# Kernel tuning notes

Hardware: AMD Instinct MI355X
Metric: run time of the kernel (lower is better)

The kernel has to match this reference:

```python
import jax, jax.numpy as jnp
import numpy as np

P, B, H, IN, L = 64, 256, 512, 2, 2


def setup_inputs() -> dict:
    key = jax.random.key(0)
    ks = jax.random.split(key, 16)
    s = 1.0 / np.sqrt(H)
    inp = {
        'input_traces': jax.random.normal(ks[0], (B, P, IN), jnp.float32),
        'h0': jax.random.normal(ks[1], (P, L, B, H), jnp.float32) * 0.1,
        'c0': jax.random.normal(ks[2], (P, L, B, H), jnp.float32) * 0.1,
        # layer 0 LSTM params (PyTorch layout: [4H, in] with gate order i,f,g,o)
        'w_ih0': jax.random.uniform(ks[3], (4 * H, IN), jnp.float32, -s, s),
        'w_hh0': jax.random.uniform(ks[4], (4 * H, H), jnp.float32, -s, s),
        'b_ih0': jax.random.uniform(ks[5], (4 * H,), jnp.float32, -s, s),
        'b_hh0': jax.random.uniform(ks[6], (4 * H,), jnp.float32, -s, s),
        # layer 1 LSTM params
        'w_ih1': jax.random.uniform(ks[7], (4 * H, H), jnp.float32, -s, s),
        'w_hh1': jax.random.uniform(ks[8], (4 * H, H), jnp.float32, -s, s),
        'b_ih1': jax.random.uniform(ks[9], (4 * H,), jnp.float32, -s, s),
        'b_hh1': jax.random.uniform(ks[10], (4 * H,), jnp.float32, -s, s),
    }
    return inp


def _lstm_forward(input_traces, h0, c0, params):
    # Fuse pedestrian and batch dims into one big batch PB = P*B; the original
    # loops over pedestrians calling the SAME LSTM weights, so this is exact.
    x = jnp.transpose(input_traces, (1, 0, 2)).reshape(P * B, IN)  # [PB, 2]
    h = jnp.transpose(h0, (1, 0, 2, 3)).reshape(L, P * B, H)       # [L, PB, H]
    c = jnp.transpose(c0, (1, 0, 2, 3)).reshape(L, P * B, H)
    h_next, c_next = [], []
    for l in range(L):
        wi, wh, bi, bh = params[l]
        gates = x @ wi.T + bi + h[l] @ wh.T + bh                   # [PB, 4H]
        ig, fg, gg, og = jnp.split(gates, 4, axis=-1)
        ig, fg, og = jax.nn.sigmoid(ig), jax.nn.sigmoid(fg), jax.nn.sigmoid(og)
        gg = jnp.tanh(gg)
        c_new = fg * c[l] + ig * gg
        h_new = og * jnp.tanh(c_new)
        h_next.append(h_new)
        c_next.append(c_new)
        x = h_new
    out = x.reshape(P, B, H).transpose(1, 0, 2)                    # [B, P, H]
    hn = jnp.stack(h_next).reshape(L, P, B, H).transpose(1, 0, 2, 3)
    cn = jnp.stack(c_next).reshape(L, P, B, H).transpose(1, 0, 2, 3)
    return out, hn, cn


def reference(input_traces, h0, c0, w_ih0, w_hh0, b_ih0, b_hh0,
              w_ih1, w_hh1, b_ih1, b_hh1):
    params = [(w_ih0, w_hh0, b_ih0, b_hh0), (w_ih1, w_hh1, b_ih1, b_hh1)]
    return _lstm_forward(input_traces, h0, c0, params)
```

## Files before the change

kernel.cpp:

```cpp
#include <hip/hip_runtime.h>
#include <hip/hip_bf16.h>

#define PP 64
#define BB 256
#define HH 512
#define MM (PP * BB)

#define HN_BASE (BB * PP * HH)
#define CN_BASE (HN_BASE + PP * 2 * BB * HH)

typedef __attribute__((ext_vector_type(8))) short bf16x8;
typedef __attribute__((ext_vector_type(4))) float floatx4;

__device__ __forceinline__ float sigf(float x) { return 1.0f / (1.0f + __expf(-x)); }
__device__ __forceinline__ float tanh_(float x) { return 2.0f / (1.0f + __expf(-2.0f * x)) - 1.0f; }

__device__ __forceinline__ short f2bf(float f) {
  unsigned u = __float_as_uint(f);
  u = (u + 0x7FFFu + ((u >> 16) & 1u)) >> 16;
  return (short)u;
}

template <typename T>
__device__ __forceinline__ float tofl(T v);
template <> __device__ __forceinline__ float tofl<float>(float v) { return v; }
template <> __device__ __forceinline__ float tofl<__hip_bfloat16>(__hip_bfloat16 v) { return __bfloat162float(v); }

template <typename T>
__device__ __forceinline__ T fromfl(float v);
template <> __device__ __forceinline__ float fromfl<float>(float v) { return v; }
template <> __device__ __forceinline__ __hip_bfloat16 fromfl<__hip_bfloat16>(float v) { return __float2bfloat16(v); }

template <typename T>
__device__ __forceinline__ bf16x8 load8(const T* p);
template <> __device__ __forceinline__ bf16x8 load8<__hip_bfloat16>(const __hip_bfloat16* p) {
  return *(const bf16x8*)p;
}
template <> __device__ __forceinline__ bf16x8 load8<float>(const float* p) {
  float4 f0 = *(const float4*)p;
  float4 f1 = *((const float4*)p + 1);
  bf16x8 v;
  v[0] = f2bf(f0.x); v[1] = f2bf(f0.y); v[2] = f2bf(f0.z); v[3] = f2bf(f0.w);
  v[4] = f2bf(f1.x); v[5] = f2bf(f1.y); v[6] = f2bf(f1.z); v[7] = f2bf(f1.w);
  return v;
}

__device__ __forceinline__ bool detect_f32(const void* w_ih0) {
  const unsigned short* p = (const unsigned short*)w_ih0;
  int l = threadIdx.x & 63;
  unsigned short a = p[2 * l], b = p[2 * l + 1];
  int big = ((a & 0x7F80) >= 0x3F80) || ((b & 0x7F80) >= 0x3F80);
  return __any(big);
}

template <typename T, int LAYER>
__device__ __forceinline__ void lstm_body(
    const T* __restrict__ xin, const T* __restrict__ h0, const T* __restrict__ c0,
    const T* __restrict__ wih, const T* __restrict__ whh,
    const T* __restrict__ bih, const T* __restrict__ bhh,
    T* out, __hip_bfloat16* ldsA, __hip_bfloat16* ldsW)
{
  const int tid  = threadIdx.x;
  const int nb   = blockIdx.x;
  const int hb   = blockIdx.y;
  const int lane = tid & 63;
  const int wid  = tid >> 6;
  const int quad = lane >> 4;
  const int lrow = lane & 15;
  const int p0   = nb >> 1;

  floatx4 acc[4][4];
#pragma unroll
  for (int g = 0; g < 4; ++g)
#pragma unroll
    for (int mi = 0; mi < 4; ++mi)
#pragma unroll
      for (int q = 0; q < 4; ++q) acc[g][mi][q] = 0.0f;

  int arow[4], wrow[4];
#pragma unroll
  for (int mi = 0; mi < 4; ++mi) arow[mi] = (wid >> 1) * 64 + mi * 16 + lrow;
#pragma unroll
  for (int g = 0; g < 4; ++g) wrow[g] = g * 32 + (wid & 1) * 16 + lrow;

  const int sr = tid >> 3;
  const int sc = tid & 7;

  const int KITERS = (LAYER == 0) ? 8 : 16;

  for (int kt = 0; kt < KITERS; ++kt) {
    bf16x8 ra[4], rw[4];
#pragma unroll
    for (int round = 0; round < 4; ++round) {
      int r = sr + round * 32;
      int b = ((nb & 1) << 7) + r;
      const T* srcA;
      if (LAYER == 0) {
        srcA = h0 + ((size_t)((p0 * 2) * 256 + b)) * 512 + kt * 64 + sc * 8;
      } else {
        if (kt < 8)
          srcA = out + HN_BASE + ((size_t)((p0 * 2) * 256 + b)) * 512 + kt * 64 + sc * 8;
        else
          srcA = h0 + ((size_t)((p0 * 2 + 1) * 256 + b)) * 512 + (kt - 8) * 64 + sc * 8;
      }
      ra[round] = load8<T>(srcA);

      int j = (r >> 5) * 512 + hb * 32 + (r & 31);
      const T* srcW;
      if (LAYER == 0) {
        srcW = whh + (size_t)j * 512 + kt * 64 + sc * 8;
      } else {
        if (kt < 8) srcW = wih + (size_t)j * 512 + kt * 64 + sc * 8;
        else        srcW = whh + (size_t)j * 512 + (kt - 8) * 64 + sc * 8;
      }
      rw[round] = load8<T>(srcW);
    }

    __syncthreads();
#pragma unroll
    for (int round = 0; round < 4; ++round) {
      int r = sr + round * 32;
      int p = sc ^ (r & 7);
      *(bf16x8*)((char*)ldsA + r * 128 + p * 16) = ra[round];
      *(bf16x8*)((char*)ldsW + r * 128 + p * 16) = rw[round];
    }
    __syncthreads();

#pragma unroll
    for (int ks = 0; ks < 2; ++ks) {
      bf16x8 aF[4], wF[4];
#pragma unroll
      for (int mi = 0; mi < 4; ++mi) {
        int ch = (ks * 4 + quad) ^ (arow[mi] & 7);
        aF[mi] = *(const bf16x8*)((const char*)ldsA + arow[mi] * 128 + ch * 16);
      }
#pragma unroll
      for (int g = 0; g < 4; ++g) {
        int ch = (ks * 4 + quad) ^ (wrow[g] & 7);
        wF[g] = *(const bf16x8*)((const char*)ldsW + wrow[g] * 128 + ch * 16);
      }
#pragma unroll
      for (int g = 0; g < 4; ++g)
#pragma unroll
        for (int mi = 0; mi < 4; ++mi)
          acc[g][mi] = __builtin_amdgcn_mfma_f32_16x16x32_bf16(
              aF[mi], wF[g], acc[g][mi], 0, 0, 0);
    }
  }

  const int hloc = hb * 32 + (wid & 1) * 16 + lrow;
  float bias[4], wx0[4], wx1[4];
#pragma unroll
  for (int g = 0; g < 4; ++g) {
    int j = g * 512 + hloc;
    bias[g] = tofl<T>(bih[j]) + tofl<T>(bhh[j]);
    if (LAYER == 0) {
      wx0[g] = tofl<T>(wih[j * 2]);
      wx1[g] = tofl<T>(wih[j * 2 + 1]);
    }
  }
  const int crow0 = (p0 * 2 + LAYER) * 256;
#pragma unroll
  for (int mi = 0; mi < 4; ++mi) {
#pragma unroll
    for (int r = 0; r < 4; ++r) {
      int b = ((nb & 1) << 7) + (wid >> 1) * 64 + mi * 16 + quad * 4 + r;
      float gv0 = acc[0][mi][r] + bias[0];
      float gv1 = acc[1][mi][r] + bias[1];
      float gv2 = acc[2][mi][r] + bias[2];
      float gv3 = acc[3][mi][r] + bias[3];
      if (LAYER == 0) {
        float x0 = tofl<T>(xin[(b * 64 + p0) * 2]);
        float x1 = tofl<T>(xin[(b * 64 + p0) * 2 + 1]);
        gv0 += x0 * wx0[0] + x1 * wx1[0];
        gv1 += x0 * wx0[1] + x1 * wx1[1];
        gv2 += x0 * wx0[2] + x1 * wx1[2];
        gv3 += x0 * wx0[3] + x1 * wx1[3];
      }
      float ig = sigf(gv0), fg = sigf(gv1);
      float gg = tanh_(gv2), og = sigf(gv3);
      size_t ro = ((size_t)(crow0 + b)) * 512 + hloc;
      float co   = tofl<T>(c0[ro]);
      float cnew = fg * co + ig * gg;
      float hnew = og * tanh_(cnew);
      out[HN_BASE + ro] = fromfl<T>(hnew);
      out[CN_BASE + ro] = fromfl<T>(cnew);
      if (LAYER == 1)
        out[(size_t)(b * 64 + p0) * 512 + hloc] = fromfl<T>(hnew);
    }
  }
}

template <int LAYER>
__global__ void __launch_bounds__(256)
lstm_layer(const void* xin, const void* h0, const void* c0,
           const void* wih, const void* whh, const void* bih, const void* bhh,
           const void* w_ih0_detect, void* out)
{
  __shared__ __align__(16) __hip_bfloat16 ldsA[128 * 64];
  __shared__ __align__(16) __hip_bfloat16 ldsW[128 * 64];
  if (detect_f32(w_ih0_detect)) {
    lstm_body<float, LAYER>((const float*)xin, (const float*)h0, (const float*)c0,
                            (const float*)wih, (const float*)whh,
                            (const float*)bih, (const float*)bhh,
                            (float*)out, ldsA, ldsW);
  } else {
    lstm_body<__hip_bfloat16, LAYER>((const __hip_bfloat16*)xin, (const __hip_bfloat16*)h0,
                                     (const __hip_bfloat16*)c0, (const __hip_bfloat16*)wih,
                                     (const __hip_bfloat16*)whh, (const __hip_bfloat16*)bih,
                                     (const __hip_bfloat16*)bhh, (__hip_bfloat16*)out,
                                     ldsA, ldsW);
  }
}

extern "C" void kernel_launch(void* const* d_in, const int* in_sizes, int n_in,
                              void* d_out, int out_size, void* d_ws, size_t ws_size,
                              hipStream_t stream) {
  dim3 grid(MM / 128, HH / 32);
  dim3 block(256);
  lstm_layer<0><<<grid, block, 0, stream>>>(d_in[0], d_in[1], d_in[2],
                                            d_in[3], d_in[4], d_in[5], d_in[6],
                                            d_in[3], d_out);
  lstm_layer<1><<<grid, block, 0, stream>>>(d_in[0], d_in[1], d_in[2],
                                            d_in[7], d_in[8], d_in[9], d_in[10],
                                            d_in[3], d_out);
}
```

Baseline: 523.4 us.

## Pre-pack h0 and weights into bf16 swizzled tiles in workspace

Adds prep kernels that convert h0 and the recurrent/input weights to bf16 and lay them out as contiguous pre-swizzled 16KB tiles in the workspace. The GEMM kernels then read those tiles directly, coalesced and without per-iteration fp32-to-bf16 conversion, and prefetch the next k-tile into registers while the current one is computed. Layer 0 also writes its h output as bf16 straight into the tile layout layer 1 consumes. This removes repeated fp32 loads and conversions across the 16 h-blocks, at the cost of two extra launches and workspace traffic; the new path only runs if the workspace is large enough.

```diff
diff --git a/kernel.cpp b/kernel.cpp
--- a/kernel.cpp
+++ b/kernel.cpp
@@ -8,6 +8,15 @@
 
 #define HN_BASE (BB * PP * HH)
 #define CN_BASE (HN_BASE + PP * 2 * BB * HH)
+
+#define TILE_BYTES 16384
+#define WS_A0   0ull
+#define WS_A1A  16777216ull
+#define WS_A1B  33554432ull
+#define WS_W0   50331648ull
+#define WS_W1A  52428800ull
+#define WS_W1B  54525952ull
+#define WS_NEED 56623104ull
 
 typedef __attribute__((ext_vector_type(8))) short bf16x8;
 typedef __attribute__((ext_vector_type(4))) float floatx4;
@@ -51,6 +60,229 @@
   unsigned short a = p[2 * l], b = p[2 * l + 1];
   int big = ((a & 0x7F80) >= 0x3F80) || ((b & 0x7F80) >= 0x3F80);
   return __any(big);
+}
+
+
+template <typename T>
+__device__ __forceinline__ void prep_A_body(const T* __restrict__ h0, char* __restrict__ ws) {
+  const int pb = blockIdx.x, kt = blockIdx.y, l = blockIdx.z;
+  char* dst = ws + (l ? WS_A1B : WS_A0) + ((size_t)(pb * 8 + kt)) * TILE_BYTES;
+  const int ped = pb >> 1, bh = pb & 1;
+  const T* src = h0 + ((size_t)(ped * 2 + l) * 256) * 512;
+  const int tid = threadIdx.x;
+#pragma unroll
+  for (int i = 0; i < 4; ++i) {
+    int idx = i * 256 + tid;
+    int r = idx >> 3;
+    int p = idx & 7;
+    int c = p ^ (r & 7);
+    *(bf16x8*)(dst + (size_t)idx * 16) =
+        load8<T>(src + (size_t)(bh * 128 + r) * 512 + kt * 64 + c * 8);
+  }
+}
+
+__global__ void __launch_bounds__(256) prep_A_k(const void* h0, const void* det, void* ws) {
+  if (detect_f32(det)) prep_A_body<float>((const float*)h0, (char*)ws);
+  else prep_A_body<__hip_bfloat16>((const __hip_bfloat16*)h0, (char*)ws);
+}
+
+template <typename T>
+__device__ __forceinline__ void prep_W_body(const T* __restrict__ w0, const T* __restrict__ w1a,
+                                            const T* __restrict__ w1b, char* __restrict__ ws) {
+  const int m = blockIdx.x >> 4, hb = blockIdx.x & 15, kt = blockIdx.y;
+  const T* src = (m == 0) ? w0 : (m == 1 ? w1a : w1b);
+  const size_t base = (m == 0) ? WS_W0 : (m == 1 ? WS_W1A : WS_W1B);
+  char* dst = ws + base + ((size_t)(hb * 8 + kt)) * TILE_BYTES;
+  const int tid = threadIdx.x;
+#pragma unroll
+  for (int i = 0; i < 4; ++i) {
+    int idx = i * 256 + tid;
+    int r = idx >> 3;
+    int p = idx & 7;
+    int c = p ^ (r & 7);
+    int j = (r >> 5) * 512 + hb * 32 + (r & 31);
+    *(bf16x8*)(dst + (size_t)idx * 16) =
+        load8<T>(src + (size_t)j * 512 + kt * 64 + c * 8);
+  }
+}
+
+__global__ void __launch_bounds__(256) prep_W_k(const void* w0, const void* w1a, const void* w1b,
+                                                const void* det, void* ws) {
+  if (detect_f32(det)) prep_W_body<float>((const float*)w0, (const float*)w1a, (const float*)w1b, (char*)ws);
+  else prep_W_body<__hip_bfloat16>((const __hip_bfloat16*)w0, (const __hip_bfloat16*)w1a,
+                                   (const __hip_bfloat16*)w1b, (char*)ws);
+}
+
+template <typename T, int LAYER>
+__device__ __forceinline__ void lstm_ws_body(
+    const T* __restrict__ xin, const T* __restrict__ c0,
+    const T* __restrict__ wih, const T* __restrict__ bih, const T* __restrict__ bhh,
+    T* __restrict__ out, char* __restrict__ ws,
+    char* __restrict__ ldsA, char* __restrict__ ldsW)
+{
+  const int tid  = threadIdx.x;
+  const int nb   = blockIdx.x;
+  const int hb   = blockIdx.y;
+  const int lane = tid & 63;
+  const int wid  = tid >> 6;
+  const int quad = lane >> 4;
+  const int lrow = lane & 15;
+  const int p0   = nb >> 1;
+
+  floatx4 acc[4][4];
+#pragma unroll
+  for (int g = 0; g < 4; ++g)
+#pragma unroll
+    for (int mi = 0; mi < 4; ++mi)
+#pragma unroll
+      for (int q = 0; q < 4; ++q) acc[g][mi][q] = 0.0f;
+
+  int arow[4], wrow[4];
+#pragma unroll
+  for (int mi = 0; mi < 4; ++mi) arow[mi] = (wid >> 1) * 64 + mi * 16 + lrow;
+#pragma unroll
+  for (int g = 0; g < 4; ++g) wrow[g] = g * 32 + (wid & 1) * 16 + lrow;
+
+  constexpr int KITERS = (LAYER == 0) ? 8 : 16;
+
+  auto tileptr = [&](int kt, const char*& at, const char*& wt) {
+    if (LAYER == 0) {
+      at = ws + WS_A0  + ((size_t)(nb * 8 + kt)) * TILE_BYTES;
+      wt = ws + WS_W0  + ((size_t)(hb * 8 + kt)) * TILE_BYTES;
+    } else if (kt < 8) {
+      at = ws + WS_A1A + ((size_t)(nb * 8 + kt)) * TILE_BYTES;
+      wt = ws + WS_W1A + ((size_t)(hb * 8 + kt)) * TILE_BYTES;
+    } else {
+      at = ws + WS_A1B + ((size_t)(nb * 8 + kt - 8)) * TILE_BYTES;
+      wt = ws + WS_W1B + ((size_t)(hb * 8 + kt - 8)) * TILE_BYTES;
+    }
+  };
+
+  bf16x8 rA[4], rW[4];
+  {
+    const char *at, *wt;
+    tileptr(0, at, wt);
+#pragma unroll
+    for (int i = 0; i < 4; ++i) {
+      int off = (i * 256 + tid) * 16;
+      rA[i] = *(const bf16x8*)(at + off);
+      rW[i] = *(const bf16x8*)(wt + off);
+    }
+  }
+
+  for (int kt = 0; kt < KITERS; ++kt) {
+    __syncthreads();
+#pragma unroll
+    for (int i = 0; i < 4; ++i) {
+      int off = (i * 256 + tid) * 16;
+      *(bf16x8*)(ldsA + off) = rA[i];
+      *(bf16x8*)(ldsW + off) = rW[i];
+    }
+    __syncthreads();
+
+    if (kt + 1 < KITERS) {
+      const char *at, *wt;
+      tileptr(kt + 1, at, wt);
+#pragma unroll
+      for (int i = 0; i < 4; ++i) {
+        int off = (i * 256 + tid) * 16;
+        rA[i] = *(const bf16x8*)(at + off);
+        rW[i] = *(const bf16x8*)(wt + off);
+      }
+    }
+
+#pragma unroll
+    for (int ks = 0; ks < 2; ++ks) {
+      bf16x8 aF[4], wF[4];
+#pragma unroll
+      for (int mi = 0; mi < 4; ++mi) {
+        int ch = (ks * 4 + quad) ^ (arow[mi] & 7);
+        aF[mi] = *(const bf16x8*)(ldsA + arow[mi] * 128 + ch * 16);
+      }
+#pragma unroll
+      for (int g = 0; g < 4; ++g) {
+        int ch = (ks * 4 + quad) ^ (wrow[g] & 7);
+        wF[g] = *(const bf16x8*)(ldsW + wrow[g] * 128 + ch * 16);
+      }
+#pragma unroll
+      for (int g = 0; g < 4; ++g)
+#pragma unroll
+        for (int mi = 0; mi < 4; ++mi)
+          acc[g][mi] = __builtin_amdgcn_mfma_f32_16x16x32_bf16(
+              aF[mi], wF[g], acc[g][mi], 0, 0, 0);
+    }
+  }
+
+  const int hloc = hb * 32 + (wid & 1) * 16 + lrow;
+  float bias[4], wx0[4], wx1[4];
+#pragma unroll
+  for (int g = 0; g < 4; ++g) {
+    int j = g * 512 + hloc;
+    bias[g] = tofl<T>(bih[j]) + tofl<T>(bhh[j]);
+    if (LAYER == 0) {
+      wx0[g] = tofl<T>(wih[j * 2]);
+      wx1[g] = tofl<T>(wih[j * 2 + 1]);
+    }
+  }
+  const int crow0 = (p0 * 2 + LAYER) * 256;
+  const int kt_h = hloc >> 6;
+  const int cl   = (hloc >> 3) & 7;
+  const int wib  = hloc & 7;
+  char* a1a_tile = ws + WS_A1A + ((size_t)(nb * 8 + kt_h)) * TILE_BYTES;
+
+#pragma unroll
+  for (int mi = 0; mi < 4; ++mi) {
+#pragma unroll
+    for (int r = 0; r < 4; ++r) {
+      int rr = (wid >> 1) * 64 + mi * 16 + quad * 4 + r;
+      int b  = ((nb & 1) << 7) + rr;
+      float gv0 = acc[0][mi][r] + bias[0];
+      float gv1 = acc[1][mi][r] + bias[1];
+      float gv2 = acc[2][mi][r] + bias[2];
+      float gv3 = acc[3][mi][r] + bias[3];
+      if (LAYER == 0) {
+        float x0 = tofl<T>(xin[(b * 64 + p0) * 2]);
+        float x1 = tofl<T>(xin[(b * 64 + p0) * 2 + 1]);
+        gv0 += x0 * wx0[0] + x1 * wx1[0];
+        gv1 += x0 * wx0[1] + x1 * wx1[1];
+        gv2 += x0 * wx0[2] + x1 * wx1[2];
+        gv3 += x0 * wx0[3] + x1 * wx1[3];
+      }
+      float ig = sigf(gv0), fg = sigf(gv1);
+      float gg = tanh_(gv2), og = sigf(gv3);
+      size_t ro = ((size_t)(crow0 + b)) * 512 + hloc;
+      float co   = tofl<T>(c0[ro]);
+      float cnew = fg * co + ig * gg;
+      float hnew = og * tanh_(cnew);
+      out[HN_BASE + ro] = fromfl<T>(hnew);
+      out[CN_BASE + ro] = fromfl<T>(cnew);
+      if (LAYER == 0) {
+        *(short*)(a1a_tile + rr * 128 + ((cl ^ (rr & 7)) * 16) + wib * 2) = f2bf(hnew);
+      }
+      if (LAYER == 1)
+        out[(size_t)(b * 64 + p0) * 512 + hloc] = fromfl<T>(hnew);
+    }
+  }
+}
+
+template <int LAYER>
+__global__ void __launch_bounds__(256)
+lstm_ws(const void* xin, const void* c0, const void* wih,
+        const void* bih, const void* bhh, const void* det,
+        void* out, void* ws)
+{
+  __shared__ __align__(16) char ldsA[TILE_BYTES];
+  __shared__ __align__(16) char ldsW[TILE_BYTES];
+  if (detect_f32(det)) {
+    lstm_ws_body<float, LAYER>((const float*)xin, (const float*)c0, (const float*)wih,
+                               (const float*)bih, (const float*)bhh,
+                               (float*)out, (char*)ws, ldsA, ldsW);
+  } else {
+    lstm_ws_body<__hip_bfloat16, LAYER>((const __hip_bfloat16*)xin, (const __hip_bfloat16*)c0,
+                                        (const __hip_bfloat16*)wih, (const __hip_bfloat16*)bih,
+                                        (const __hip_bfloat16*)bhh,
+                                        (__hip_bfloat16*)out, (char*)ws, ldsA, ldsW);
+  }
 }
 
 template <typename T, int LAYER>
@@ -85,7 +317,6 @@
 
   const int sr = tid >> 3;
   const int sc = tid & 7;
-
   const int KITERS = (LAYER == 0) ? 8 : 16;
 
   for (int kt = 0; kt < KITERS; ++kt) {
@@ -216,12 +447,22 @@
 extern "C" void kernel_launch(void* const* d_in, const int* in_sizes, int n_in,
                               void* d_out, int out_size, void* d_ws, size_t ws_size,
                               hipStream_t stream) {
-  dim3 grid(MM / 128, HH / 32);
   dim3 block(256);
-  lstm_layer<0><<<grid, block, 0, stream>>>(d_in[0], d_in[1], d_in[2],
-                                            d_in[3], d_in[4], d_in[5], d_in[6],
-                                            d_in[3], d_out);
-  lstm_layer<1><<<grid, block, 0, stream>>>(d_in[0], d_in[1], d_in[2],
-                                            d_in[7], d_in[8], d_in[9], d_in[10],
-                                            d_in[3], d_out);
-}
+  if (d_ws != nullptr && ws_size >= WS_NEED) {
+    prep_A_k<<<dim3(128, 8, 2), block, 0, stream>>>(d_in[1], d_in[3], d_ws);
+    prep_W_k<<<dim3(48, 8), block, 0, stream>>>(d_in[4], d_in[7], d_in[8], d_in[3], d_ws);
+    dim3 grid(MM / 128, HH / 32);
+    lstm_ws<0><<<grid, block, 0, stream>>>(d_in[0], d_in[2], d_in[3],
+                                           d_in[5], d_in[6], d_in[3], d_out, d_ws);
+    lstm_ws<1><<<grid, block, 0, stream>>>(d_in[0], d_in[2], d_in[3],
+                                           d_in[9], d_in[10], d_in[3], d_out, d_ws);
+  } else {
+    dim3 grid(MM / 128, HH / 32);
+    lstm_layer<0><<<grid, block, 0, stream>>>(d_in[0], d_in[1], d_in[2],
+                                              d_in[3], d_in[4], d_in[5], d_in[6],
+                                              d_in[3], d_out);
+    lstm_layer<1><<<grid, block, 0, stream>>>(d_in[0], d_in[1], d_in[2],
+                                              d_in[7], d_in[8], d_in[9], d_in[10],
+                                              d_in[3], d_out);
+  }
+}
```

Result: faster. 500.2 us (-4.4%).
